# Kernel tuning notes

Hardware: AMD Instinct MI355X
Metric: run time of the kernel (lower is better)

The kernel has to match this reference:

```python
import jax, jax.numpy as jnp
import numpy as np

NUM_CLASSES = 2047
TIME_WEIGHT = 2.0
EOS_COEF = 0.1
B, Q, N = 64, 100, 16


def _lsa(cost):
    """Jonker-Volgenant min-cost assignment for rectangular cost [R, C], R <= C.
    Returns (row_ind, col_ind) with row_ind = arange(R). Equivalent to
    scipy.optimize.linear_sum_assignment."""
    R, Cn = cost.shape
    u = np.zeros(R + 1)
    v = np.zeros(Cn + 1)
    p = np.zeros(Cn + 1, dtype=np.int64)  # p[j] = 1-based row matched to col j (0 = free)
    for i in range(1, R + 1):
        p[0] = i
        j0 = 0
        minv = np.full(Cn + 1, np.inf)
        used = np.zeros(Cn + 1, dtype=bool)
        way = np.zeros(Cn + 1, dtype=np.int64)
        while True:
            used[j0] = True
            i0 = p[j0]
            cur = cost[i0 - 1] - u[i0] - v[1:]
            free = ~used[1:]
            upd = free & (cur < minv[1:])
            minv[1:] = np.where(upd, cur, minv[1:])
            way[1:] = np.where(upd, j0, way[1:])
            j1 = int(np.argmin(np.where(free, minv[1:], np.inf))) + 1
            delta = minv[j1]
            u[p[used]] += delta
            v[used] -= delta
            minv[1:] = np.where(free, minv[1:] - delta, minv[1:])
            j0 = j1
            if p[j0] == 0:
                break
        while j0 != 0:  # augment along the alternating path
            j1 = way[j0]
            p[j0] = p[j1]
            j0 = j1
    col4row = np.zeros(R, dtype=np.int64)
    for j in range(1, Cn + 1):
        if p[j] > 0:
            col4row[p[j] - 1] = j - 1
    return np.arange(R), col4row


def _match(C):
    """C: np.ndarray [B, Q, N]. Returns (query_idx [B,N], target_idx [B,N])."""
    b, q, n = C.shape
    qs = np.zeros((b, n), np.int64)
    ts = np.zeros((b, n), np.int64)
    for i in range(b):
        r, c = _lsa(C[i].T)  # rows = targets (N), cols = queries (Q); N <= Q
        ts[i] = r
        qs[i] = c
    return qs, ts


def setup_inputs() -> dict:
    key = jax.random.key(0)
    k1, k2, k3, k4 = jax.random.split(key, 4)
    pred_logits = jax.random.normal(k1, (B, Q, NUM_CLASSES + 1), dtype=jnp.float32)
    pred_time = jax.random.uniform(k2, (B, Q, 1), dtype=jnp.float32)
    labels = jax.random.randint(k3, (B, N), 1, NUM_CLASSES + 1)  # class 0 = no-object
    timestamps = jax.random.uniform(k4, (B, N, 1), dtype=jnp.float32)
    return {"pred_logits": pred_logits, "pred_time": pred_time,
            "labels": labels, "timestamps": timestamps}


def reference(pred_logits, pred_time, labels, timestamps):
    b, q = pred_logits.shape[:2]
    n = labels.shape[1]
    # --- Hungarian matching cost (detached, host-side assignment as in the original) ---
    probs = jax.nn.softmax(pred_logits, axis=-1)                              # [B,Q,C+1]
    cost_class = -jnp.take_along_axis(probs, labels[:, None, :], axis=2)      # [B,Q,N]
    cost_time = jnp.abs(pred_time[..., 0][:, :, None] -
                        timestamps[..., 0][:, None, :])                       # [B,Q,N] (cdist p=1)
    C = cost_class + TIME_WEIGHT * cost_time
    Cnp = np.nan_to_num(np.asarray(jax.device_get(C)),
                        nan=100.0, posinf=100.0, neginf=-100.0)
    qs, ts = _match(Cnp)
    qs_j = jnp.asarray(qs)  # matched query indices  [B,N]
    ts_j = jnp.asarray(ts)  # matched target indices [B,N]
    # --- weighted cross entropy over all queries ---
    class_ids = jnp.take_along_axis(labels, ts_j, axis=1)                     # [B,N]
    batch_ar = jnp.arange(b)[:, None]
    target_classes = jnp.zeros((b, q), dtype=jnp.int64).at[batch_ar, qs_j].set(class_ids)
    logZ = jax.nn.logsumexp(pred_logits, axis=-1)                             # [B,Q]
    tgt_logit = jnp.take_along_axis(pred_logits, target_classes[..., None], axis=2)[..., 0]
    nll = logZ - tgt_logit                                                    # [B,Q]
    ce_w = jnp.ones(NUM_CLASSES + 1, jnp.float32).at[0].set(EOS_COEF)
    w = ce_w[target_classes]
    loss_ce = jnp.sum(w * nll) / jnp.sum(w)
    # --- L1 loss on matched timestamps ---
    matched_pred = pred_time[batch_ar, qs_j, 0]                               # [B,N]
    matched_tgt = jnp.take_along_axis(timestamps[..., 0], ts_j, axis=1)       # [B,N]
    loss_time = jnp.mean(jnp.abs(matched_pred - matched_tgt))
    return loss_ce + TIME_WEIGHT * loss_time
```

## Files before the change

kernel.cpp:

```cpp
#include <hip/hip_runtime.h>
#include <hip/hip_bf16.h>
#include <math.h>

#define BB 64
#define QQ 100
#define NN 16
#define CC 2048
#define TIME_WEIGHT 2.0f
#define EOS_COEF 0.1f

__device__ __forceinline__ double readlane_d(double x, int lane) {
    int lo = __builtin_amdgcn_readlane(__double2loint(x), lane);
    int hi = __builtin_amdgcn_readlane(__double2hiint(x), lane);
    return __hiloint2double(hi, lo);
}

__global__ __launch_bounds__(256) void lse_cost_kernel(
    const float* __restrict__ logits, const float* __restrict__ ptime,
    const int* __restrict__ labels, const float* __restrict__ tstamp,
    float* __restrict__ logZ, float* __restrict__ Cg,
    float* __restrict__ lsepart, float* __restrict__ sums, int* __restrict__ counter)
{
    if (blockIdx.x == 0 && threadIdx.x == 0) {
        sums[0] = 0.f; sums[1] = 0.f; *counter = 0;
    }
    const int wave = threadIdx.x >> 6;
    const int lane = threadIdx.x & 63;
    const int bq = blockIdx.x * 4 + wave;
    const int b = bq / QQ, q = bq % QQ;
    const float4* row4 = (const float4*)(logits + (size_t)bq * CC);

    float4 v[8];
    #pragma unroll
    for (int c = 0; c < 8; ++c) v[c] = row4[c * 64 + lane];

    float m = -INFINITY;
    #pragma unroll
    for (int c = 0; c < 8; ++c)
        m = fmaxf(m, fmaxf(fmaxf(v[c].x, v[c].y), fmaxf(v[c].z, v[c].w)));
    #pragma unroll
    for (int s = 1; s < 64; s <<= 1) m = fmaxf(m, __shfl_xor(m, s, 64));

    float sum = 0.f;
    #pragma unroll
    for (int c = 0; c < 8; ++c)
        sum += expf(v[c].x - m) + expf(v[c].y - m) +
               expf(v[c].z - m) + expf(v[c].w - m);
    #pragma unroll
    for (int s = 1; s < 64; s <<= 1) sum += __shfl_xor(sum, s, 64);

    const float lz = m + logf(sum);
    if (lane == 0) logZ[bq] = lz;

    const float pt = ptime[bq];
    if (lane < NN) {
        int lab = labels[b * NN + lane];
        float lg = logits[(size_t)bq * CC + lab];
        float cc = -expf(lg - lz);
        float ct = fabsf(pt - tstamp[b * NN + lane]);
        float val = cc + TIME_WEIGHT * ct;
        if (isnan(val)) val = 100.0f;
        else if (isinf(val)) val = (val > 0.f) ? 100.0f : -100.0f;
        Cg[((size_t)b * NN + lane) * QQ + q] = val;
    }

    __shared__ float red[4];
    if (lane == 0) red[wave] = lz - logits[(size_t)bq * CC];
    __syncthreads();
    if (threadIdx.x == 0)
        lsepart[blockIdx.x] = red[0] + red[1] + red[2] + red[3];
}

__global__ __launch_bounds__(64) void hungarian_kernel(
    const float* __restrict__ Cg, const float* __restrict__ logits,
    const float* __restrict__ ptime, const int* __restrict__ labels,
    const float* __restrict__ tstamp, const float* __restrict__ logZ,
    const float* __restrict__ lsepart, float* __restrict__ sums,
    int* __restrict__ counter, float* __restrict__ out)
{
    const int b = blockIdx.x;
    const int t = threadIdx.x;

    __shared__ double cost[NN * QQ];
    __shared__ int qsl[NN];

    for (int idx = t; idx < NN * QQ; idx += 64)
        cost[idx] = (double)Cg[(size_t)b * NN * QQ + idx];
    __syncthreads();

    const int jc0 = t + 1;
    const int jc1 = t + 65;
    const bool has2 = (jc1 <= QQ);
    double v0 = 0.0, v1 = 0.0;
    double ureg = 0.0;
    int preg0 = 0, preg1 = 0;
    const double INF = __builtin_inf();

    for (int i = 1; i <= NN; ++i) {
        double minv0 = INF, minv1 = INF;
        bool used0 = false, used1 = false;
        int way0 = 0, way1 = 0;
        bool inTree = (t == i - 1);
        int j0 = 0;
        int i0 = i;

        while (true) {
            used0 |= (j0 == jc0);
            used1 |= (j0 == jc1);
            inTree = inTree || (t == i0 - 1);
            const double u_i0 = readlane_d(ureg, i0 - 1);
            const double* crow = &cost[(i0 - 1) * QQ];

            if (!used0) {
                double cur = crow[jc0 - 1] - u_i0 - v0;
                if (cur < minv0) { minv0 = cur; way0 = j0; }
            }
            if (has2 && !used1) {
                double cur = crow[jc1 - 1] - u_i0 - v1;
                if (cur < minv1) { minv1 = cur; way1 = j0; }
            }

            double m0 = used0 ? INF : minv0;
            double m1 = (has2 && !used1) ? minv1 : INF;
            double gmin = fmin(m0, m1);
            #pragma unroll
            for (int s = 1; s < 32; s <<= 1)
                gmin = fmin(gmin, __shfl_xor(gmin, s, 64));
            {
                double h0 = readlane_d(gmin, 0);
                double h1 = readlane_d(gmin, 32);
                gmin = fmin(h0, h1);
            }
            unsigned long long A  = __ballot(!used0 && (minv0 == gmin));
            unsigned long long Bm = __ballot(has2 && !used1 && (minv1 == gmin));
            int j1 = (A != 0ull) ? ((int)__builtin_ctzll(A) + 1)
                                 : ((int)__builtin_ctzll(Bm) + 65);
            const double delta = gmin;

            if (inTree) ureg += delta;
            if (used0) v0 -= delta; else minv0 -= delta;
            if (has2) { if (used1) v1 -= delta; else minv1 -= delta; }

            j0 = j1;
            int pj = (j0 <= 64) ? __builtin_amdgcn_readlane(preg0, j0 - 1)
                                : __builtin_amdgcn_readlane(preg1, j0 - 65);
            if (pj == 0) break;
            i0 = pj;
        }

        while (j0 != 0) {
            int jn = (j0 <= 64) ? __builtin_amdgcn_readlane(way0, j0 - 1)
                                : __builtin_amdgcn_readlane(way1, j0 - 65);
            int pv;
            if (jn == 0) pv = i;
            else pv = (jn <= 64) ? __builtin_amdgcn_readlane(preg0, jn - 1)
                                 : __builtin_amdgcn_readlane(preg1, jn - 65);
            if (j0 == jc0) preg0 = pv;
            if (has2 && j0 == jc1) preg1 = pv;
            j0 = jn;
        }
    }

    if (preg0 > 0) qsl[preg0 - 1] = jc0 - 1;
    if (has2 && preg1 > 0) qsl[preg1 - 1] = jc1 - 1;
    __syncthreads();

    float corr = 0.f, tl = 0.f;
    if (t < NN) {
        int qcol = qsl[t];
        int lab = labels[b * NN + t];
        int bq = b * QQ + qcol;
        float lz = logZ[bq];
        float lgm = logits[(size_t)bq * CC + lab];
        float lg0 = logits[(size_t)bq * CC];
        corr = (lz - lgm) - EOS_COEF * (lz - lg0);
        tl = fabsf(ptime[bq] - tstamp[b * NN + t]);
    }
    #pragma unroll
    for (int s = 1; s < 64; s <<= 1) {
        corr += __shfl_xor(corr, s, 64);
        tl   += __shfl_xor(tl, s, 64);
    }

    int old = 0;
    if (t == 0) {
        atomicAdd(&sums[0], corr);
        atomicAdd(&sums[1], tl);
        __threadfence();
        old = atomicAdd(counter, 1);
    }
    old = __shfl(old, 0, 64);
    if (old == BB - 1) {
        __threadfence();
        float r0 = 0.f;
        #pragma unroll
        for (int k = 0; k < 25; ++k) r0 += lsepart[t + 64 * k];
        #pragma unroll
        for (int s = 1; s < 64; s <<= 1) r0 += __shfl_xor(r0, s, 64);
        if (t == 0) {
            float s0 = atomicAdd(&sums[0], 0.0f);
            float s1 = atomicAdd(&sums[1], 0.0f);
            const float sum_w = (float)(BB * NN) * 1.0f
                              + (float)(BB * (QQ - NN)) * EOS_COEF;
            float loss_ce = (EOS_COEF * r0 + s0) / sum_w;
            float loss_t  = s1 / (float)(BB * NN);
            out[0] = loss_ce + TIME_WEIGHT * loss_t;
        }
    }
}

extern "C" void kernel_launch(void* const* d_in, const int* in_sizes, int n_in,
                              void* d_out, int out_size, void* d_ws, size_t ws_size,
                              hipStream_t stream) {
    const float* logits = (const float*)d_in[0];
    const float* ptime  = (const float*)d_in[1];
    const int*   labels = (const int*)d_in[2];
    const float* tstamp = (const float*)d_in[3];
    float* out = (float*)d_out;

    char* ws = (char*)d_ws;
    float* logZ    = (float*)ws;
    float* Cg      = (float*)(ws + 25600);
    float* lsepart = (float*)(ws + 435200);
    float* sums    = (float*)(ws + 441600);
    int*   counter = (int*)(ws + 441608);

    lse_cost_kernel<<<1600, 256, 0, stream>>>(logits, ptime, labels, tstamp,
                                              logZ, Cg, lsepart, sums, counter);
    hungarian_kernel<<<BB, 64, 0, stream>>>(Cg, logits, ptime, labels, tstamp,
                                            logZ, lsepart, sums, counter, out);
}
```

Before: 113.2 us.

## Store cost matrix query-major and keep each column's costs in registers

The cost kernel now writes the cost matrix transposed ([B,Q,N]), so each Hungarian thread can load its two columns' 16 costs as float4 registers. This removes the shared-memory double cost table, its fill loop and the barrier, and replaces per-iteration LDS reads with register selects. The label and timestamp loads are hoisted before the reduction to overlap their latency, and the min reduction uses fewer shuffle steps plus more readlanes. The tradeoff is added register pressure and select logic in the serial inner loop.

```diff
diff --git a/kernel.cpp b/kernel.cpp
--- a/kernel.cpp
+++ b/kernel.cpp
@@ -18,7 +18,7 @@
 __global__ __launch_bounds__(256) void lse_cost_kernel(
     const float* __restrict__ logits, const float* __restrict__ ptime,
     const int* __restrict__ labels, const float* __restrict__ tstamp,
-    float* __restrict__ logZ, float* __restrict__ Cg,
+    float* __restrict__ logZ, float* __restrict__ CgT,
     float* __restrict__ lsepart, float* __restrict__ sums, int* __restrict__ counter)
 {
     if (blockIdx.x == 0 && threadIdx.x == 0) {
@@ -27,12 +27,19 @@
     const int wave = threadIdx.x >> 6;
     const int lane = threadIdx.x & 63;
     const int bq = blockIdx.x * 4 + wave;
-    const int b = bq / QQ, q = bq % QQ;
+    const int b = bq / QQ;
     const float4* row4 = (const float4*)(logits + (size_t)bq * CC);
 
     float4 v[8];
     #pragma unroll
     for (int c = 0; c < 8; ++c) v[c] = row4[c * 64 + lane];
+
+    const float pt = ptime[bq];
+    int lab = 0; float ts = 0.f;
+    if (lane < NN) {
+        lab = labels[b * NN + lane];
+        ts  = tstamp[b * NN + lane];
+    }
 
     float m = -INFINITY;
     #pragma unroll
@@ -52,16 +59,14 @@
     const float lz = m + logf(sum);
     if (lane == 0) logZ[bq] = lz;
 
-    const float pt = ptime[bq];
     if (lane < NN) {
-        int lab = labels[b * NN + lane];
         float lg = logits[(size_t)bq * CC + lab];
         float cc = -expf(lg - lz);
-        float ct = fabsf(pt - tstamp[b * NN + lane]);
+        float ct = fabsf(pt - ts);
         float val = cc + TIME_WEIGHT * ct;
         if (isnan(val)) val = 100.0f;
         else if (isinf(val)) val = (val > 0.f) ? 100.0f : -100.0f;
-        Cg[((size_t)b * NN + lane) * QQ + q] = val;
+        CgT[(size_t)bq * NN + lane] = val;
     }
 
     __shared__ float red[4];
@@ -72,7 +77,7 @@
 }
 
 __global__ __launch_bounds__(64) void hungarian_kernel(
-    const float* __restrict__ Cg, const float* __restrict__ logits,
+    const float* __restrict__ CgT, const float* __restrict__ logits,
     const float* __restrict__ ptime, const int* __restrict__ labels,
     const float* __restrict__ tstamp, const float* __restrict__ logZ,
     const float* __restrict__ lsepart, float* __restrict__ sums,
@@ -81,16 +86,19 @@
     const int b = blockIdx.x;
     const int t = threadIdx.x;
 
-    __shared__ double cost[NN * QQ];
     __shared__ int qsl[NN];
-
-    for (int idx = t; idx < NN * QQ; idx += 64)
-        cost[idx] = (double)Cg[(size_t)b * NN * QQ + idx];
-    __syncthreads();
 
     const int jc0 = t + 1;
     const int jc1 = t + 65;
     const bool has2 = (jc1 <= QQ);
+    const int t2 = has2 ? (t + 64) : t;
+
+    const float* colbase = CgT + (size_t)b * QQ * NN;
+    const float4* cp0 = (const float4*)(colbase + t * NN);
+    const float4* cp1 = (const float4*)(colbase + t2 * NN);
+    const float4 a0 = cp0[0], a1 = cp0[1], a2 = cp0[2], a3 = cp0[3];
+    const float4 b0 = cp1[0], b1 = cp1[1], b2 = cp1[2], b3 = cp1[3];
+
     double v0 = 0.0, v1 = 0.0;
     double ureg = 0.0;
     int preg0 = 0, preg1 = 0;
@@ -109,14 +117,23 @@
             used1 |= (j0 == jc1);
             inTree = inTree || (t == i0 - 1);
             const double u_i0 = readlane_d(ureg, i0 - 1);
-            const double* crow = &cost[(i0 - 1) * QQ];
+
+            const int mrow = i0 - 1;
+            float4 ha = (mrow & 8) ? ((mrow & 4) ? a3 : a2)
+                                   : ((mrow & 4) ? a1 : a0);
+            float4 hb = (mrow & 8) ? ((mrow & 4) ? b3 : b2)
+                                   : ((mrow & 4) ? b1 : b0);
+            float ca = (mrow & 2) ? ((mrow & 1) ? ha.w : ha.z)
+                                  : ((mrow & 1) ? ha.y : ha.x);
+            float cb = (mrow & 2) ? ((mrow & 1) ? hb.w : hb.z)
+                                  : ((mrow & 1) ? hb.y : hb.x);
 
             if (!used0) {
-                double cur = crow[jc0 - 1] - u_i0 - v0;
+                double cur = (double)ca - u_i0 - v0;
                 if (cur < minv0) { minv0 = cur; way0 = j0; }
             }
             if (has2 && !used1) {
-                double cur = crow[jc1 - 1] - u_i0 - v1;
+                double cur = (double)cb - u_i0 - v1;
                 if (cur < minv1) { minv1 = cur; way1 = j0; }
             }
 
@@ -124,12 +141,14 @@
             double m1 = (has2 && !used1) ? minv1 : INF;
             double gmin = fmin(m0, m1);
             #pragma unroll
-            for (int s = 1; s < 32; s <<= 1)
+            for (int s = 1; s < 16; s <<= 1)
                 gmin = fmin(gmin, __shfl_xor(gmin, s, 64));
             {
                 double h0 = readlane_d(gmin, 0);
-                double h1 = readlane_d(gmin, 32);
-                gmin = fmin(h0, h1);
+                double h1 = readlane_d(gmin, 16);
+                double h2 = readlane_d(gmin, 32);
+                double h3 = readlane_d(gmin, 48);
+                gmin = fmin(fmin(h0, h1), fmin(h2, h3));
             }
             unsigned long long A  = __ballot(!used0 && (minv0 == gmin));
             unsigned long long Bm = __ballot(has2 && !used1 && (minv1 == gmin));
@@ -220,13 +239,13 @@
 
     char* ws = (char*)d_ws;
     float* logZ    = (float*)ws;
-    float* Cg      = (float*)(ws + 25600);
+    float* CgT     = (float*)(ws + 25600);
     float* lsepart = (float*)(ws + 435200);
     float* sums    = (float*)(ws + 441600);
     int*   counter = (int*)(ws + 441608);
 
     lse_cost_kernel<<<1600, 256, 0, stream>>>(logits, ptime, labels, tstamp,
-                                              logZ, Cg, lsepart, sums, counter);
-    hungarian_kernel<<<BB, 64, 0, stream>>>(Cg, logits, ptime, labels, tstamp,
+                                              logZ, CgT, lsepart, sums, counter);
+    hungarian_kernel<<<BB, 64, 0, stream>>>(CgT, logits, ptime, labels, tstamp,
                                             logZ, lsepart, sums, counter, out);
 }
```

New measurement: 115.9 us. 1.02x slower.
